# Kernel optimization log

Hardware: AMD Instinct MI355X
Metric: run time of the kernel (lower is better)

Reference implementation:

```python
import jax, jax.numpy as jnp
import numpy as np

S = 4096      # packed sequence length
DIM = 1024    # model dim
H = 8         # num heads
HD = 64       # per-branch head dim (head_dim // 2 in the module)
LAMBDA_INIT = 0.8 - 0.6 * float(np.exp(-0.3 * 0.0))  # depth=0 -> 0.2
EPS = 1e-5


def setup_inputs() -> dict:
    key = jax.random.key(0)
    ks = jax.random.split(key, 10)
    P = 2 * H * HD  # = 1024
    return {
        "x": jax.random.normal(ks[0], (S, DIM), jnp.float32),
        "mask": jnp.ones((1, 1, S, S), jnp.bool_),
        "Wq": jax.random.normal(ks[1], (DIM, P), jnp.float32) * 0.02,
        "Wk": jax.random.normal(ks[2], (DIM, P), jnp.float32) * 0.02,
        "Wv": jax.random.normal(ks[3], (DIM, P), jnp.float32) * 0.02,
        "Wo": jax.random.normal(ks[4], (P, DIM), jnp.float32) * 0.02,
        "lambda_q1": jax.random.normal(ks[5], (HD,), jnp.float32) * 0.1,
        "lambda_k1": jax.random.normal(ks[6], (HD,), jnp.float32) * 0.1,
        "lambda_q2": jax.random.normal(ks[7], (HD,), jnp.float32) * 0.1,
        "lambda_k2": jax.random.normal(ks[8], (HD,), jnp.float32) * 0.1,
        "subln_weight": jnp.ones((2 * HD,), jnp.float32),
    }


def reference(x, mask, Wq, Wk, Wv, Wo, lambda_q1, lambda_k1, lambda_q2,
              lambda_k2, subln_weight):
    # projections: (S, 2H, HD) split into branch index along a new axis
    xq = (x @ Wq).reshape(S, H, 2, HD)   # [2*H] view -> (H,2) contiguous split
    xk = (x @ Wk).reshape(S, H, 2, HD)
    xv = (x @ Wv).reshape(S, H, 2 * HD)
    q1, q2 = xq[:, :, 0], xq[:, :, 1]    # (S,H,HD)
    k1, k2 = xk[:, :, 0], xk[:, :, 1]

    scale = 1.0 / jnp.sqrt(jnp.float32(HD))
    bias = jnp.where(mask[0, 0], 0.0, -jnp.inf)  # (S,S) additive mask

    def sdpa(q, k):
        # q,k: (S,H,HD); xv: (S,H,2HD)
        scores = jnp.einsum('shd,thd->hst', q, k) * scale + bias  # (H,S,S)
        p = jax.nn.softmax(scores, axis=-1)
        return jnp.einsum('hst,thd->shd', p, xv)                  # (S,H,2HD)

    attn1 = sdpa(q1, k1)
    attn2 = sdpa(q2, k2)

    lam1 = jnp.exp(jnp.sum(lambda_q1 * lambda_k1))
    lam2 = jnp.exp(jnp.sum(lambda_q2 * lambda_k2))
    lambda_full = lam1 - lam2 + LAMBDA_INIT

    attn = attn1 - lambda_full * attn2                            # (S,H,2HD)
    # RMSNorm over last dim (2*HD) with learnable weight
    attn = attn * jax.lax.rsqrt(jnp.mean(attn * attn, axis=-1, keepdims=True) + EPS)
    attn = attn * subln_weight
    attn = attn * (1.0 - LAMBDA_INIT)
    return attn.reshape(S, H * 2 * HD) @ Wo                       # (S, DIM)
```

## Files before the change

### kernel.cpp

```cpp
#include <hip/hip_runtime.h>
#include <hip/hip_bf16.h>
#include <type_traits>
#include <utility>


using bf16 = __hip_bfloat16;

static constexpr int SQ = 4096;
static constexpr int DM = 1024;
static constexpr float LAMB_INIT = 0.2f;
static constexpr float KSC = 0.18033688011112043f;

typedef float  f32x4    __attribute__((ext_vector_type(4)));
typedef short  s16x4    __attribute__((ext_vector_type(4)));
typedef short  bf16x8_i __attribute__((ext_vector_type(8)));
typedef __bf16 bf16x8_b __attribute__((ext_vector_type(8)));

template<typename T, typename = void> struct mfma_ok : std::false_type {};
template<typename T> struct mfma_ok<T, std::void_t<decltype(
    __builtin_amdgcn_mfma_f32_16x16x32_bf16(std::declval<T>(), std::declval<T>(),
                                            std::declval<f32x4>(), 0, 0, 0))>>
    : std::true_type {};
using abfrag = std::conditional_t<mfma_ok<bf16x8_b>::value, bf16x8_b, bf16x8_i>;

__device__ __forceinline__ f32x4 mfma16(abfrag a, abfrag b, f32x4 c) {
    return __builtin_amdgcn_mfma_f32_16x16x32_bf16(a, b, c, 0, 0, 0);
}
__device__ __forceinline__ abfrag ldfrag(const bf16* p) {
    return *reinterpret_cast<const abfrag*>(p);
}
__device__ __forceinline__ short bf2s(bf16 b) {
    short s; __builtin_memcpy(&s, &b, 2); return s;
}
__device__ __forceinline__ float fexp2(float x) {
#if __has_builtin(__builtin_amdgcn_exp2f)
    return __builtin_amdgcn_exp2f(x);
#else
    return exp2f(x);
#endif
}
__device__ __forceinline__ int cvtpk(float lo, float hi) {
    int r;
    asm("v_cvt_pk_bf16_f32 %0, %1, %2" : "=v"(r) : "v"(lo), "v"(hi));
    return r;
}
__device__ __forceinline__ void gld_lds16(const bf16* g, bf16* l) {
    __builtin_amdgcn_global_load_lds((__attribute__((address_space(1))) void*)g,
                                     (__attribute__((address_space(3))) void*)l,
                                     16, 0, 0);
}


__global__ __launch_bounds__(256) void convert_x(const float* __restrict__ in,
                                                 bf16* __restrict__ outp)
{
    const size_t i = ((size_t)blockIdx.x * 256 + threadIdx.x) * 4;
    const f32x4 v = *reinterpret_cast<const f32x4*>(in + i);
    s16x4 o;
#pragma unroll
    for (int j = 0; j < 4; ++j) o[j] = bf2s(__float2bfloat16(v[j]));
    *reinterpret_cast<s16x4*>(outp + i) = o;
}

__global__ __launch_bounds__(256) void transpose_w(
    const float* __restrict__ Wq, const float* __restrict__ Wk,
    const float* __restrict__ Wv, const float* __restrict__ Wo,
    bf16* __restrict__ Wqt, bf16* __restrict__ Wkt,
    bf16* __restrict__ Wvt, bf16* __restrict__ Wot)
{
    const int z = blockIdx.z;
    const float* src = (z == 0) ? Wq : (z == 1) ? Wk : (z == 2) ? Wv : Wo;
    bf16* dst        = (z == 0) ? Wqt : (z == 1) ? Wkt : (z == 2) ? Wvt : Wot;
    const float scale = (z == 0) ? KSC : 1.0f;
    __shared__ float tbuf[32][33];
    const int k0 = blockIdx.x * 32, n0 = blockIdx.y * 32;
    const int c = threadIdx.x & 31, r0 = threadIdx.x >> 5;
#pragma unroll
    for (int i = 0; i < 4; ++i)
        tbuf[r0 + i * 8][c] = src[(size_t)(k0 + r0 + i * 8) * 1024 + n0 + c];
    __syncthreads();
#pragma unroll
    for (int i = 0; i < 4; ++i)
        dst[(size_t)(n0 + r0 + i * 8) * 1024 + k0 + c] =
            __float2bfloat16(tbuf[c][r0 + i * 8] * scale);
}

__global__ __launch_bounds__(256) void transpose_v(const bf16* __restrict__ V,
                                                   bf16* __restrict__ Vt)
{
    __shared__ bf16 tbuf[32][33];
    const int s0 = blockIdx.x * 32, n0 = blockIdx.y * 32;
    const int c = threadIdx.x & 31, r0 = threadIdx.x >> 5;
#pragma unroll
    for (int i = 0; i < 4; ++i)
        tbuf[r0 + i * 8][c] = V[(size_t)(s0 + r0 + i * 8) * 1024 + n0 + c];
    __syncthreads();
#pragma unroll
    for (int i = 0; i < 4; ++i)
        Vt[(size_t)(n0 + r0 + i * 8) * 4096 + s0 + c] = tbuf[c][r0 + i * 8];
}

__global__ void lambda_kernel(const float* lq1, const float* lk1,
                              const float* lq2, const float* lk2, float* outp)
{
    const int lane = threadIdx.x;
    float a = lq1[lane] * lk1[lane];
    float b = lq2[lane] * lk2[lane];
#pragma unroll
    for (int m = 1; m < 64; m <<= 1) {
        a += __shfl_xor(a, m, 64);
        b += __shfl_xor(b, m, 64);
    }
    if (lane == 0) outp[0] = __expf(a) - __expf(b) + LAMB_INIT;
}


template<bool BF16OUT>
__device__ __forceinline__ void gemm_core(const bf16* __restrict__ A,
                                          const bf16* __restrict__ Bt,
                                          void* __restrict__ Cout,
                                          int m0, int n0, int ldc)
{
    __shared__ __align__(16) bf16 As[128 * 32];
    __shared__ __align__(16) bf16 Bs[128 * 32];
    const int tid  = threadIdx.x;
    const int wid  = tid >> 6;
    const int lane = tid & 63;
    const int l15  = lane & 15;
    const int l4   = lane >> 4;
    const int wr   = wid >> 1;
    const int wc   = wid & 1;

    const f32x4 zero4 = {0.f, 0.f, 0.f, 0.f};
    f32x4 acc[4][4];
#pragma unroll
    for (int i = 0; i < 4; ++i)
#pragma unroll
        for (int j = 0; j < 4; ++j) acc[i][j] = zero4;

    for (int kt = 0; kt < 1024; kt += 32) {
        __syncthreads();
#pragma unroll
        for (int it = 0; it < 2; ++it) {
            const int flat = it * 256 + tid;
            const int row  = flat >> 2;
            const int c16  = flat & 3;
            const int ldst = (it * 256 + wid * 64) * 8;
            gld_lds16(&A [(size_t)(m0 + row) * 1024 + kt + c16 * 8], &As[ldst]);
            gld_lds16(&Bt[(size_t)(n0 + row) * 1024 + kt + c16 * 8], &Bs[ldst]);
        }
        __syncthreads();
        abfrag a[4], b[4];
#pragma unroll
        for (int mi = 0; mi < 4; ++mi)
            a[mi] = ldfrag(&As[(wr * 64 + mi * 16 + l15) * 32 + l4 * 8]);
#pragma unroll
        for (int ni = 0; ni < 4; ++ni)
            b[ni] = ldfrag(&Bs[(wc * 64 + ni * 16 + l15) * 32 + l4 * 8]);
#pragma unroll
        for (int mi = 0; mi < 4; ++mi)
#pragma unroll
            for (int ni = 0; ni < 4; ++ni)
                acc[mi][ni] = mfma16(a[mi], b[ni], acc[mi][ni]);
    }

#pragma unroll
    for (int mi = 0; mi < 4; ++mi)
#pragma unroll
        for (int ni = 0; ni < 4; ++ni)
#pragma unroll
            for (int r = 0; r < 4; ++r) {
                const int row = m0 + wr * 64 + mi * 16 + l4 * 4 + r;
                const int col = n0 + wc * 64 + ni * 16 + l15;
                if constexpr (BF16OUT)
                    ((bf16*)Cout)[(size_t)row * ldc + col] = __float2bfloat16(acc[mi][ni][r]);
                else
                    ((float*)Cout)[(size_t)row * ldc + col] = acc[mi][ni][r];
            }
}

__global__ __launch_bounds__(256, 2) void gemm_qkv(
    const bf16* __restrict__ xbf,
    const bf16* __restrict__ Wqt, const bf16* __restrict__ Wkt,
    const bf16* __restrict__ Wvt,
    bf16* __restrict__ Qo, bf16* __restrict__ Ko, bf16* __restrict__ Vo)
{
    const int which = blockIdx.y >> 3;
    const bf16* Bt = (which == 0) ? Wqt : (which == 1) ? Wkt : Wvt;
    bf16* Cp       = (which == 0) ? Qo  : (which == 1) ? Ko  : Vo;
    gemm_core<true>(xbf, Bt, Cp, blockIdx.x * 128, (blockIdx.y & 7) * 128, 1024);
}

__global__ __launch_bounds__(256, 2) void gemm_out(
    const bf16* __restrict__ Amat, const bf16* __restrict__ Wot,
    float* __restrict__ out)
{
    gemm_core<false>(Amat, Wot, out, blockIdx.x * 128, blockIdx.y * 128, 1024);
}


__global__ __launch_bounds__(512, 2) void flash_diff(
    const bf16* __restrict__ Qm, const bf16* __restrict__ Km,
    const bf16* __restrict__ Vtm, const float* __restrict__ lam_ptr,
    const float* __restrict__ subln, bf16* __restrict__ Amat)
{
    const int bid  = blockIdx.x;
    const int h    = bid & 7;
    const int qt   = bid >> 3;
    const int tid  = threadIdx.x;
    const int wid  = tid >> 6;
    const int lane = tid & 63;
    const int l15  = lane & 15;
    const int l4   = lane >> 4;
    const int qbase = qt * 128 + wid * 16;
    const int swz   = (l15 & 7) << 4;

    constexpr float THR = 8.0f;
    constexpr int KOFF = 0, VOFF = 49152, BUFSZ = 16384;

    __shared__ __align__(16) char smem[98304];

    abfrag qf[2][2];
#pragma unroll
    for (int c = 0; c < 2; ++c)
#pragma unroll
        for (int kc = 0; kc < 2; ++kc)
            qf[c][kc] = ldfrag(&Qm[(size_t)(qbase + l15) * DM +
                                   h * 128 + c * 64 + kc * 32 + l4 * 8]);
    asm volatile("" :: "v"(qf[0][0]), "v"(qf[0][1]), "v"(qf[1][0]), "v"(qf[1][1]));

    union { abfrag f; short s[8]; } uon;
#pragma unroll
    for (int i = 0; i < 8; ++i) uon.s[i] = (short)0x3F80;
    const abfrag ones = uon.f;

    const bf16* kap[2];
    const bf16* vap[2];
#pragma unroll
    for (int it = 0; it < 2; ++it) {
        const int slot = it * 512 + tid;
        const int krow = slot >> 4;
        const int kcb  = ((slot & 15) << 4) ^ ((krow & 7) << 4);
        kap[it] = Km + (size_t)krow * DM + h * 128 + (kcb >> 1);
        const int vrow = slot >> 3;
        const int vcb  = ((slot & 7) << 4) ^ ((vrow & 7) << 4);
        vap[it] = Vtm + (size_t)(h * 128 + vrow) * SQ + (vcb >> 1);
    }
    auto stage = [&](int buf) {
        char* kd = smem + KOFF + buf * BUFSZ;
        char* vd = smem + VOFF + buf * BUFSZ;
#pragma unroll
        for (int it = 0; it < 2; ++it) {
            gld_lds16(kap[it], (bf16*)(kd + (it * 512 + wid * 64) * 16));
            kap[it] += 64 * DM;
            gld_lds16(vap[it], (bf16*)(vd + (it * 512 + wid * 64) * 16));
            vap[it] += 64;
        }
    };

    const int kLane0 = l15 * 256 + ((l4 * 16) ^ swz);
    const int kLane1 = l15 * 256 + ((64 + l4 * 16) ^ swz);
    int vLane[4];
#pragma unroll
    for (int ch = 0; ch < 2; ++ch)
#pragma unroll
        for (int hh = 0; hh < 2; ++hh)
            vLane[ch * 2 + hh] = l15 * 128 + ((ch * 64 + hh * 32 + l4 * 8) ^ swz);

    const f32x4 zero4 = {0.f, 0.f, 0.f, 0.f};
    f32x4 o_[2][8];
#pragma unroll
    for (int c = 0; c < 2; ++c)
#pragma unroll
        for (int vt = 0; vt < 8; ++vt) o_[c][vt] = zero4;
    f32x4 lacc[2] = {zero4, zero4};
    float m_loc[2] = {0.f, 0.f};

    stage(0);
    stage(1);
    asm volatile("s_waitcnt vmcnt(4)" ::: "memory");
    __builtin_amdgcn_s_barrier();

    int cur = 0, nxt = 2;
    constexpr int NT = SQ / 64;
#pragma unroll 1
    for (int t = 0; t < NT; ++t) {
        const bool pf = (t + 2 < NT);
        if (pf) stage(nxt);

        const char* kbuf = smem + KOFF + cur * BUFSZ;
        const char* vbuf = smem + VOFF + cur * BUFSZ;
        const char* kb0  = kbuf + kLane0;
        const char* kb1  = kbuf + kLane1;

        abfrag pa[2][2];
#pragma unroll
        for (int c = 0; c < 2; ++c) {
            const float mc = m_loc[c];
            const f32x4 binit = {-mc, -mc, -mc, -mc};
            f32x4 sc[4];
#pragma unroll
            for (int j = 0; j < 4; ++j) {
                const abfrag k0 = *(const abfrag*)(kb0 + (j * 4096 + c * 128));
                const abfrag k1 = *(const abfrag*)(kb1 + (j * 4096 + c * 128));
                f32x4 z = mfma16(k0, qf[c][0], binit);
                sc[j] = mfma16(k1, qf[c][1], z);
            }
            float lmx = fmaxf(fmaxf(sc[0][0], sc[0][1]), fmaxf(sc[0][2], sc[0][3]));
#pragma unroll
            for (int j = 1; j < 4; ++j)
                lmx = fmaxf(lmx, fmaxf(fmaxf(sc[j][0], sc[j][1]),
                                       fmaxf(sc[j][2], sc[j][3])));
            if (__any(lmx > THR)) {
                float mx = lmx;
                mx = fmaxf(mx, __shfl_xor(mx, 16, 64));
                mx = fmaxf(mx, __shfl_xor(mx, 32, 64));
                const float alpha = fexp2(-mx);
                m_loc[c] += mx;
#pragma unroll
                for (int r = 0; r < 4; ++r) {
                    const float alr = __shfl(alpha, l4 * 4 + r, 64);
#pragma unroll
                    for (int vt = 0; vt < 8; ++vt) o_[c][vt][r] *= alr;
                    lacc[c][r] *= alr;
                }
#pragma unroll
                for (int j = 0; j < 4; ++j)
#pragma unroll
                    for (int r = 0; r < 4; ++r) sc[j][r] -= mx;
            }
            f32x4 pe[4];
#pragma unroll
            for (int j = 0; j < 4; ++j)
#pragma unroll
                for (int r = 0; r < 4; ++r) pe[j][r] = fexp2(sc[j][r]);
            union { abfrag f; int i[4]; } u0, u1;
            u0.i[0] = cvtpk(pe[0][0], pe[0][1]);
            u0.i[1] = cvtpk(pe[0][2], pe[0][3]);
            u0.i[2] = cvtpk(pe[1][0], pe[1][1]);
            u0.i[3] = cvtpk(pe[1][2], pe[1][3]);
            u1.i[0] = cvtpk(pe[2][0], pe[2][1]);
            u1.i[1] = cvtpk(pe[2][2], pe[2][3]);
            u1.i[2] = cvtpk(pe[3][0], pe[3][1]);
            u1.i[3] = cvtpk(pe[3][2], pe[3][3]);
            pa[c][0] = u0.f;
            pa[c][1] = u1.f;
        }

        const char* vb00 = vbuf + vLane[0];
        const char* vb01 = vbuf + vLane[1];
        const char* vb10 = vbuf + vLane[2];
        const char* vb11 = vbuf + vLane[3];

        __builtin_amdgcn_s_setprio(1);
        lacc[0] = mfma16(pa[0][0], ones, lacc[0]);
        lacc[0] = mfma16(pa[0][1], ones, lacc[0]);
        lacc[1] = mfma16(pa[1][0], ones, lacc[1]);
        lacc[1] = mfma16(pa[1][1], ones, lacc[1]);
#pragma unroll
        for (int vt = 0; vt < 8; ++vt) {
            union { abfrag f; s16x4 hh[2]; } v0, v1;
            v0.hh[0] = *(const s16x4*)(vb00 + vt * 2048);
            v0.hh[1] = *(const s16x4*)(vb01 + vt * 2048);
            v1.hh[0] = *(const s16x4*)(vb10 + vt * 2048);
            v1.hh[1] = *(const s16x4*)(vb11 + vt * 2048);
            o_[0][vt] = mfma16(pa[0][0], v0.f, o_[0][vt]);
            o_[1][vt] = mfma16(pa[1][0], v0.f, o_[1][vt]);
            o_[0][vt] = mfma16(pa[0][1], v1.f, o_[0][vt]);
            o_[1][vt] = mfma16(pa[1][1], v1.f, o_[1][vt]);
        }
        __builtin_amdgcn_s_setprio(0);

        if (pf) asm volatile("s_waitcnt vmcnt(4)" ::: "memory");
        else    asm volatile("s_waitcnt vmcnt(0)" ::: "memory");
        __builtin_amdgcn_s_barrier();
        cur = (cur == 2) ? 0 : cur + 1;
        nxt = (nxt == 2) ? 0 : nxt + 1;
    }

    const float lam = lam_ptr[0];
    float il1[4], il2[4];
#pragma unroll
    for (int r = 0; r < 4; ++r) {
        il1[r] = 1.f / lacc[0][r];
        il2[r] = lam / lacc[1][r];
    }
#pragma unroll
    for (int r = 0; r < 4; ++r) {
        float comb[8];
        float ss = 0.f;
#pragma unroll
        for (int vt = 0; vt < 8; ++vt) {
            const float v = o_[0][vt][r] * il1[r] - o_[1][vt][r] * il2[r];
            comb[vt] = v;
            ss += v * v;
        }
        ss += __shfl_xor(ss, 1, 64);
        ss += __shfl_xor(ss, 2, 64);
        ss += __shfl_xor(ss, 4, 64);
        ss += __shfl_xor(ss, 8, 64);
        const float rinv = rsqrtf(ss * (1.f / 128.f) + 1e-5f);
        const int row = qbase + l4 * 4 + r;
#pragma unroll
        for (int vt = 0; vt < 8; ++vt) {
            const float outv = comb[vt] * rinv * subln[vt * 16 + l15] * 0.8f;
            Amat[(size_t)row * DM + h * 128 + vt * 16 + l15] = __float2bfloat16(outv);
        }
    }
}


extern "C" void kernel_launch(void* const* d_in, const int* in_sizes, int n_in,
                              void* d_out, int out_size, void* d_ws, size_t ws_size,
                              hipStream_t stream)
{
    (void)in_sizes; (void)n_in; (void)out_size; (void)ws_size;
    const float* x    = (const float*)d_in[0];
    const float* Wq   = (const float*)d_in[2];
    const float* Wk   = (const float*)d_in[3];
    const float* Wv   = (const float*)d_in[4];
    const float* Wo   = (const float*)d_in[5];
    const float* lq1  = (const float*)d_in[6];
    const float* lk1  = (const float*)d_in[7];
    const float* lq2  = (const float*)d_in[8];
    const float* lk2  = (const float*)d_in[9];
    const float* subw = (const float*)d_in[10];

    char* ws = (char*)d_ws;
    size_t off = 0;
    auto take = [&](size_t n) { void* p = ws + off; off += (n + 255) & ~(size_t)255; return p; };
    bf16* xbf = (bf16*)take((size_t)SQ * DM * 2);
    bf16* Wqt = (bf16*)take((size_t)DM * DM * 2);
    bf16* Wkt = (bf16*)take((size_t)DM * DM * 2);
    bf16* Wvt = (bf16*)take((size_t)DM * DM * 2);
    bf16* Wot = (bf16*)take((size_t)DM * DM * 2);
    bf16* Qb  = (bf16*)take((size_t)SQ * DM * 2);
    bf16* Kb  = (bf16*)take((size_t)SQ * DM * 2);
    bf16* Vb  = (bf16*)take((size_t)SQ * DM * 2);
    bf16* Vtb = (bf16*)take((size_t)SQ * DM * 2);
    bf16* Am  = (bf16*)take((size_t)SQ * DM * 2);
    float* lamp = (float*)take(256);

    convert_x   <<<dim3(SQ * DM / 1024), dim3(256), 0, stream>>>(x, xbf);
    transpose_w <<<dim3(32, 32, 4),      dim3(256), 0, stream>>>(Wq, Wk, Wv, Wo, Wqt, Wkt, Wvt, Wot);
    lambda_kernel<<<dim3(1),             dim3(64),  0, stream>>>(lq1, lk1, lq2, lk2, lamp);
    gemm_qkv    <<<dim3(32, 24),         dim3(256), 0, stream>>>(xbf, Wqt, Wkt, Wvt, Qb, Kb, Vb);
    transpose_v <<<dim3(128, 32),        dim3(256), 0, stream>>>(Vb, Vtb);
    flash_diff  <<<dim3(256),            dim3(512), 0, stream>>>(Qb, Kb, Vtb, lamp, subw, Am);
    gemm_out    <<<dim3(32, 8),          dim3(256), 0, stream>>>(Am, Wot, (float*)d_out);
}
```

Before: 192.8 us.

## Split differential attention branches across separate waves in flash kernel

Each block now runs 16 waves instead of 8. Each pair of waves shares a 16-row query slice, and each wave of the pair handles one of the two attention branches (q1/k1 or q2/k2), so it holds half the accumulators. Each thread now issues one K and one V staging load per tile instead of two. Branch 2's normalized output is handed to branch 1's wave through LDS for the final combine and RMSNorm. This cuts per-wave register pressure and serial work to gain latency hiding, at the cost of an extra LDS exchange, a block-wide sync, and a launch bound of 1024 threads with min 4 blocks that may force register spills.

```diff
diff --git a/kernel.cpp b/kernel.cpp
--- a/kernel.cpp
+++ b/kernel.cpp
@@ -199,7 +199,7 @@
 }
 
 
-__global__ __launch_bounds__(512, 2) void flash_diff(
+__global__ __launch_bounds__(1024, 4) void flash_diff(
     const bf16* __restrict__ Qm, const bf16* __restrict__ Km,
     const bf16* __restrict__ Vtm, const float* __restrict__ lam_ptr,
     const float* __restrict__ subln, bf16* __restrict__ Amat)
@@ -212,7 +212,9 @@
     const int lane = tid & 63;
     const int l15  = lane & 15;
     const int l4   = lane >> 4;
-    const int qbase = qt * 128 + wid * 16;
+    const int qw   = wid >> 1;
+    const int cw   = wid & 1;
+    const int qbase = qt * 128 + qw * 16;
     const int swz   = (l15 & 7) << 4;
 
     constexpr float THR = 8.0f;
@@ -220,46 +222,34 @@
 
     __shared__ __align__(16) char smem[98304];
 
-    abfrag qf[2][2];
-#pragma unroll
-    for (int c = 0; c < 2; ++c)
-#pragma unroll
-        for (int kc = 0; kc < 2; ++kc)
-            qf[c][kc] = ldfrag(&Qm[(size_t)(qbase + l15) * DM +
-                                   h * 128 + c * 64 + kc * 32 + l4 * 8]);
-    asm volatile("" :: "v"(qf[0][0]), "v"(qf[0][1]), "v"(qf[1][0]), "v"(qf[1][1]));
+    abfrag qf[2];
+#pragma unroll
+    for (int kc = 0; kc < 2; ++kc)
+        qf[kc] = ldfrag(&Qm[(size_t)(qbase + l15) * DM +
+                            h * 128 + cw * 64 + kc * 32 + l4 * 8]);
+    asm volatile("" :: "v"(qf[0]), "v"(qf[1]));
 
     union { abfrag f; short s[8]; } uon;
 #pragma unroll
     for (int i = 0; i < 8; ++i) uon.s[i] = (short)0x3F80;
     const abfrag ones = uon.f;
 
-    const bf16* kap[2];
-    const bf16* vap[2];
-#pragma unroll
-    for (int it = 0; it < 2; ++it) {
-        const int slot = it * 512 + tid;
-        const int krow = slot >> 4;
-        const int kcb  = ((slot & 15) << 4) ^ ((krow & 7) << 4);
-        kap[it] = Km + (size_t)krow * DM + h * 128 + (kcb >> 1);
-        const int vrow = slot >> 3;
-        const int vcb  = ((slot & 7) << 4) ^ ((vrow & 7) << 4);
-        vap[it] = Vtm + (size_t)(h * 128 + vrow) * SQ + (vcb >> 1);
-    }
+    const int krow = tid >> 4;
+    const int kcb  = ((tid & 15) << 4) ^ ((krow & 7) << 4);
+    const bf16* kap = Km + (size_t)krow * DM + h * 128 + (kcb >> 1);
+    const int vrow = tid >> 3;
+    const int vcb  = ((tid & 7) << 4) ^ ((vrow & 7) << 4);
+    const bf16* vap = Vtm + (size_t)(h * 128 + vrow) * SQ + (vcb >> 1);
+
     auto stage = [&](int buf) {
-        char* kd = smem + KOFF + buf * BUFSZ;
-        char* vd = smem + VOFF + buf * BUFSZ;
-#pragma unroll
-        for (int it = 0; it < 2; ++it) {
-            gld_lds16(kap[it], (bf16*)(kd + (it * 512 + wid * 64) * 16));
-            kap[it] += 64 * DM;
-            gld_lds16(vap[it], (bf16*)(vd + (it * 512 + wid * 64) * 16));
-            vap[it] += 64;
-        }
+        gld_lds16(kap, (bf16*)(smem + KOFF + buf * BUFSZ + wid * 1024));
+        kap += 64 * DM;
+        gld_lds16(vap, (bf16*)(smem + VOFF + buf * BUFSZ + wid * 1024));
+        vap += 64;
     };
 
-    const int kLane0 = l15 * 256 + ((l4 * 16) ^ swz);
-    const int kLane1 = l15 * 256 + ((64 + l4 * 16) ^ swz);
+    const int kLane0 = l15 * 256 + ((l4 * 16) ^ swz) + cw * 128;
+    const int kLane1 = l15 * 256 + ((64 + l4 * 16) ^ swz) + cw * 128;
     int vLane[4];
 #pragma unroll
     for (int ch = 0; ch < 2; ++ch)
@@ -268,17 +258,15 @@
             vLane[ch * 2 + hh] = l15 * 128 + ((ch * 64 + hh * 32 + l4 * 8) ^ swz);
 
     const f32x4 zero4 = {0.f, 0.f, 0.f, 0.f};
-    f32x4 o_[2][8];
-#pragma unroll
-    for (int c = 0; c < 2; ++c)
-#pragma unroll
-        for (int vt = 0; vt < 8; ++vt) o_[c][vt] = zero4;
-    f32x4 lacc[2] = {zero4, zero4};
-    float m_loc[2] = {0.f, 0.f};
+    f32x4 o_[8];
+#pragma unroll
+    for (int vt = 0; vt < 8; ++vt) o_[vt] = zero4;
+    f32x4 lacc = zero4;
+    float m_loc = 0.f;
 
     stage(0);
     stage(1);
-    asm volatile("s_waitcnt vmcnt(4)" ::: "memory");
+    asm volatile("s_waitcnt vmcnt(2)" ::: "memory");
     __builtin_amdgcn_s_barrier();
 
     int cur = 0, nxt = 2;
@@ -293,47 +281,46 @@
         const char* kb0  = kbuf + kLane0;
         const char* kb1  = kbuf + kLane1;
 
-        abfrag pa[2][2];
-#pragma unroll
-        for (int c = 0; c < 2; ++c) {
-            const float mc = m_loc[c];
-            const f32x4 binit = {-mc, -mc, -mc, -mc};
-            f32x4 sc[4];
-#pragma unroll
-            for (int j = 0; j < 4; ++j) {
-                const abfrag k0 = *(const abfrag*)(kb0 + (j * 4096 + c * 128));
-                const abfrag k1 = *(const abfrag*)(kb1 + (j * 4096 + c * 128));
-                f32x4 z = mfma16(k0, qf[c][0], binit);
-                sc[j] = mfma16(k1, qf[c][1], z);
+        const float mc = m_loc;
+        const f32x4 binit = {-mc, -mc, -mc, -mc};
+        f32x4 sc[4];
+#pragma unroll
+        for (int j = 0; j < 4; ++j) {
+            const abfrag k0 = *(const abfrag*)(kb0 + j * 4096);
+            const abfrag k1 = *(const abfrag*)(kb1 + j * 4096);
+            f32x4 z = mfma16(k0, qf[0], binit);
+            sc[j] = mfma16(k1, qf[1], z);
+        }
+        float lmx = fmaxf(fmaxf(sc[0][0], sc[0][1]), fmaxf(sc[0][2], sc[0][3]));
+#pragma unroll
+        for (int j = 1; j < 4; ++j)
+            lmx = fmaxf(lmx, fmaxf(fmaxf(sc[j][0], sc[j][1]),
+                                   fmaxf(sc[j][2], sc[j][3])));
+        if (__any(lmx > THR)) {
+            float mx = lmx;
+            mx = fmaxf(mx, __shfl_xor(mx, 16, 64));
+            mx = fmaxf(mx, __shfl_xor(mx, 32, 64));
+            const float alpha = fexp2(-mx);
+            m_loc += mx;
+#pragma unroll
+            for (int r = 0; r < 4; ++r) {
+                const float alr = __shfl(alpha, l4 * 4 + r, 64);
+#pragma unroll
+                for (int vt = 0; vt < 8; ++vt) o_[vt][r] *= alr;
+                lacc[r] *= alr;
             }
-            float lmx = fmaxf(fmaxf(sc[0][0], sc[0][1]), fmaxf(sc[0][2], sc[0][3]));
-#pragma unroll
-            for (int j = 1; j < 4; ++j)
-                lmx = fmaxf(lmx, fmaxf(fmaxf(sc[j][0], sc[j][1]),
-                                       fmaxf(sc[j][2], sc[j][3])));
-            if (__any(lmx > THR)) {
-                float mx = lmx;
-                mx = fmaxf(mx, __shfl_xor(mx, 16, 64));
-                mx = fmaxf(mx, __shfl_xor(mx, 32, 64));
-                const float alpha = fexp2(-mx);
-                m_loc[c] += mx;
-#pragma unroll
-                for (int r = 0; r < 4; ++r) {
-                    const float alr = __shfl(alpha, l4 * 4 + r, 64);
-#pragma unroll
-                    for (int vt = 0; vt < 8; ++vt) o_[c][vt][r] *= alr;
-                    lacc[c][r] *= alr;
-                }
-#pragma unroll
-                for (int j = 0; j < 4; ++j)
-#pragma unroll
-                    for (int r = 0; r < 4; ++r) sc[j][r] -= mx;
-            }
-            f32x4 pe[4];
 #pragma unroll
             for (int j = 0; j < 4; ++j)
 #pragma unroll
-                for (int r = 0; r < 4; ++r) pe[j][r] = fexp2(sc[j][r]);
+                for (int r = 0; r < 4; ++r) sc[j][r] -= mx;
+        }
+        f32x4 pe[4];
+#pragma unroll
+        for (int j = 0; j < 4; ++j)
+#pragma unroll
+            for (int r = 0; r < 4; ++r) pe[j][r] = fexp2(sc[j][r]);
+        abfrag pa[2];
+        {
             union { abfrag f; int i[4]; } u0, u1;
             u0.i[0] = cvtpk(pe[0][0], pe[0][1]);
             u0.i[1] = cvtpk(pe[0][2], pe[0][3]);
@@ -343,8 +330,8 @@
             u1.i[1] = cvtpk(pe[2][2], pe[2][3]);
             u1.i[2] = cvtpk(pe[3][0], pe[3][1]);
             u1.i[3] = cvtpk(pe[3][2], pe[3][3]);
-            pa[c][0] = u0.f;
-            pa[c][1] = u1.f;
+            pa[0] = u0.f;
+            pa[1] = u1.f;
         }
 
         const char* vb00 = vbuf + vLane[0];
@@ -353,10 +340,8 @@
         const char* vb11 = vbuf + vLane[3];
 
         __builtin_amdgcn_s_setprio(1);
-        lacc[0] = mfma16(pa[0][0], ones, lacc[0]);
-        lacc[0] = mfma16(pa[0][1], ones, lacc[0]);
-        lacc[1] = mfma16(pa[1][0], ones, lacc[1]);
-        lacc[1] = mfma16(pa[1][1], ones, lacc[1]);
+        lacc = mfma16(pa[0], ones, lacc);
+        lacc = mfma16(pa[1], ones, lacc);
 #pragma unroll
         for (int vt = 0; vt < 8; ++vt) {
             union { abfrag f; s16x4 hh[2]; } v0, v1;
@@ -364,14 +349,12 @@
             v0.hh[1] = *(const s16x4*)(vb01 + vt * 2048);
             v1.hh[0] = *(const s16x4*)(vb10 + vt * 2048);
             v1.hh[1] = *(const s16x4*)(vb11 + vt * 2048);
-            o_[0][vt] = mfma16(pa[0][0], v0.f, o_[0][vt]);
-            o_[1][vt] = mfma16(pa[1][0], v0.f, o_[1][vt]);
-            o_[0][vt] = mfma16(pa[0][1], v1.f, o_[0][vt]);
-            o_[1][vt] = mfma16(pa[1][1], v1.f, o_[1][vt]);
+            o_[vt] = mfma16(pa[0], v0.f, o_[vt]);
+            o_[vt] = mfma16(pa[1], v1.f, o_[vt]);
         }
         __builtin_amdgcn_s_setprio(0);
 
-        if (pf) asm volatile("s_waitcnt vmcnt(4)" ::: "memory");
+        if (pf) asm volatile("s_waitcnt vmcnt(2)" ::: "memory");
         else    asm volatile("s_waitcnt vmcnt(0)" ::: "memory");
         __builtin_amdgcn_s_barrier();
         cur = (cur == 2) ? 0 : cur + 1;
@@ -379,32 +362,46 @@
     }
 
     const float lam = lam_ptr[0];
-    float il1[4], il2[4];
-#pragma unroll
-    for (int r = 0; r < 4; ++r) {
-        il1[r] = 1.f / lacc[0][r];
-        il2[r] = lam / lacc[1][r];
+    float* xch = (float*)smem;
+
+    if (cw == 1) {
+        float il2[4];
+#pragma unroll
+        for (int r = 0; r < 4; ++r) il2[r] = lam / lacc[r];
+#pragma unroll
+        for (int vt = 0; vt < 8; ++vt)
+#pragma unroll
+            for (int r = 0; r < 4; ++r)
+                xch[(qw * 16 + l4 * 4 + r) * 128 + vt * 16 + l15] =
+                    o_[vt][r] * il2[r];
     }
-#pragma unroll
-    for (int r = 0; r < 4; ++r) {
-        float comb[8];
-        float ss = 0.f;
-#pragma unroll
-        for (int vt = 0; vt < 8; ++vt) {
-            const float v = o_[0][vt][r] * il1[r] - o_[1][vt][r] * il2[r];
-            comb[vt] = v;
-            ss += v * v;
-        }
-        ss += __shfl_xor(ss, 1, 64);
-        ss += __shfl_xor(ss, 2, 64);
-        ss += __shfl_xor(ss, 4, 64);
-        ss += __shfl_xor(ss, 8, 64);
-        const float rinv = rsqrtf(ss * (1.f / 128.f) + 1e-5f);
-        const int row = qbase + l4 * 4 + r;
-#pragma unroll
-        for (int vt = 0; vt < 8; ++vt) {
-            const float outv = comb[vt] * rinv * subln[vt * 16 + l15] * 0.8f;
-            Amat[(size_t)row * DM + h * 128 + vt * 16 + l15] = __float2bfloat16(outv);
+    __syncthreads();
+    if (cw == 0) {
+        float il1[4];
+#pragma unroll
+        for (int r = 0; r < 4; ++r) il1[r] = 1.f / lacc[r];
+#pragma unroll
+        for (int r = 0; r < 4; ++r) {
+            float comb[8];
+            float ss = 0.f;
+#pragma unroll
+            for (int vt = 0; vt < 8; ++vt) {
+                const float v = o_[vt][r] * il1[r] -
+                                xch[(qw * 16 + l4 * 4 + r) * 128 + vt * 16 + l15];
+                comb[vt] = v;
+                ss += v * v;
+            }
+            ss += __shfl_xor(ss, 1, 64);
+            ss += __shfl_xor(ss, 2, 64);
+            ss += __shfl_xor(ss, 4, 64);
+            ss += __shfl_xor(ss, 8, 64);
+            const float rinv = rsqrtf(ss * (1.f / 128.f) + 1e-5f);
+            const int row = qbase + l4 * 4 + r;
+#pragma unroll
+            for (int vt = 0; vt < 8; ++vt) {
+                const float outv = comb[vt] * rinv * subln[vt * 16 + l15] * 0.8f;
+                Amat[(size_t)row * DM + h * 128 + vt * 16 + l15] = __float2bfloat16(outv);
+            }
         }
     }
 }
@@ -446,6 +443,6 @@
     lambda_kernel<<<dim3(1),             dim3(64),  0, stream>>>(lq1, lk1, lq2, lk2, lamp);
     gemm_qkv    <<<dim3(32, 24),         dim3(256), 0, stream>>>(xbf, Wqt, Wkt, Wvt, Qb, Kb, Vb);
     transpose_v <<<dim3(128, 32),        dim3(256), 0, stream>>>(Vb, Vtb);
-    flash_diff  <<<dim3(256),            dim3(512), 0, stream>>>(Qb, Kb, Vtb, lamp, subw, Am);
+    flash_diff  <<<dim3(256),            dim3(1024), 0, stream>>>(Qb, Kb, Vtb, lamp, subw, Am);
     gemm_out    <<<dim3(32, 8),          dim3(256), 0, stream>>>(Am, Wot, (float*)d_out);
 }
```

Measured after the change: 235.7 us. 22.2% more time.

## Split attention over KV halves with 32-row query tiles and a combine kernel

Applied to the files above, without the earlier changes.

Each warp of the flash kernel now handles 32 query rows instead of 16, so every K/V tile staged in shared memory feeds twice as many MFMAs. The grid stays at 256 blocks because the key sequence is split into two halves (split-K). Each block writes unnormalized partial outputs in bf16 plus per-row sums and running maxima. A new combine kernel merges the two halves, applies the lambda difference and RMSNorm, and writes the activation matrix. This adds extra global traffic for the partials, one more launch, and roughly doubled accumulator registers per thread, which risks spills at the 512-thread, 2-block launch bound.

```diff
diff --git a/kernel.cpp b/kernel.cpp
--- a/kernel.cpp
+++ b/kernel.cpp
@@ -201,18 +201,21 @@
 
 __global__ __launch_bounds__(512, 2) void flash_diff(
     const bf16* __restrict__ Qm, const bf16* __restrict__ Km,
-    const bf16* __restrict__ Vtm, const float* __restrict__ lam_ptr,
-    const float* __restrict__ subln, bf16* __restrict__ Amat)
+    const bf16* __restrict__ Vtm,
+    bf16* __restrict__ pO,
+    float* __restrict__ pL,
+    float* __restrict__ pM)
 {
     const int bid  = blockIdx.x;
     const int h    = bid & 7;
-    const int qt   = bid >> 3;
+    const int qt   = (bid >> 3) & 15;
+    const int ks   = bid >> 7;
     const int tid  = threadIdx.x;
     const int wid  = tid >> 6;
     const int lane = tid & 63;
     const int l15  = lane & 15;
     const int l4   = lane >> 4;
-    const int qbase = qt * 128 + wid * 16;
+    const int qbase = qt * 256 + wid * 32;
     const int swz   = (l15 & 7) << 4;
 
     constexpr float THR = 8.0f;
@@ -220,14 +223,16 @@
 
     __shared__ __align__(16) char smem[98304];
 
-    abfrag qf[2][2];
-#pragma unroll
-    for (int c = 0; c < 2; ++c)
-#pragma unroll
-        for (int kc = 0; kc < 2; ++kc)
-            qf[c][kc] = ldfrag(&Qm[(size_t)(qbase + l15) * DM +
-                                   h * 128 + c * 64 + kc * 32 + l4 * 8]);
-    asm volatile("" :: "v"(qf[0][0]), "v"(qf[0][1]), "v"(qf[1][0]), "v"(qf[1][1]));
+    abfrag qf[2][2][2];
+#pragma unroll
+    for (int sub = 0; sub < 2; ++sub)
+#pragma unroll
+        for (int c = 0; c < 2; ++c)
+#pragma unroll
+            for (int kc = 0; kc < 2; ++kc)
+                qf[sub][c][kc] = ldfrag(&Qm[(size_t)(qbase + sub * 16 + l15) * DM +
+                                            h * 128 + c * 64 + kc * 32 + l4 * 8]);
+    asm volatile("" :: "v"(qf[0][0][0]), "v"(qf[1][1][1]));
 
     union { abfrag f; short s[8]; } uon;
 #pragma unroll
@@ -241,10 +246,10 @@
         const int slot = it * 512 + tid;
         const int krow = slot >> 4;
         const int kcb  = ((slot & 15) << 4) ^ ((krow & 7) << 4);
-        kap[it] = Km + (size_t)krow * DM + h * 128 + (kcb >> 1);
+        kap[it] = Km + (size_t)(ks * 2048 + krow) * DM + h * 128 + (kcb >> 1);
         const int vrow = slot >> 3;
         const int vcb  = ((slot & 7) << 4) ^ ((vrow & 7) << 4);
-        vap[it] = Vtm + (size_t)(h * 128 + vrow) * SQ + (vcb >> 1);
+        vap[it] = Vtm + (size_t)(h * 128 + vrow) * SQ + ks * 2048 + (vcb >> 1);
     }
     auto stage = [&](int buf) {
         char* kd = smem + KOFF + buf * BUFSZ;
@@ -268,13 +273,15 @@
             vLane[ch * 2 + hh] = l15 * 128 + ((ch * 64 + hh * 32 + l4 * 8) ^ swz);
 
     const f32x4 zero4 = {0.f, 0.f, 0.f, 0.f};
-    f32x4 o_[2][8];
-#pragma unroll
-    for (int c = 0; c < 2; ++c)
-#pragma unroll
-        for (int vt = 0; vt < 8; ++vt) o_[c][vt] = zero4;
-    f32x4 lacc[2] = {zero4, zero4};
-    float m_loc[2] = {0.f, 0.f};
+    f32x4 o_[2][2][8];
+#pragma unroll
+    for (int sub = 0; sub < 2; ++sub)
+#pragma unroll
+        for (int c = 0; c < 2; ++c)
+#pragma unroll
+            for (int vt = 0; vt < 8; ++vt) o_[sub][c][vt] = zero4;
+    f32x4 lacc[2][2] = {{zero4, zero4}, {zero4, zero4}};
+    float m_loc[2][2] = {{0.f, 0.f}, {0.f, 0.f}};
 
     stage(0);
     stage(1);
@@ -282,7 +289,7 @@
     __builtin_amdgcn_s_barrier();
 
     int cur = 0, nxt = 2;
-    constexpr int NT = SQ / 64;
+    constexpr int NT = 2048 / 64;
 #pragma unroll 1
     for (int t = 0; t < NT; ++t) {
         const bool pf = (t + 2 < NT);
@@ -293,18 +300,20 @@
         const char* kb0  = kbuf + kLane0;
         const char* kb1  = kbuf + kLane1;
 
-        abfrag pa[2][2];
+        abfrag pa[2][2][2];
+#pragma unroll
+        for (int sub = 0; sub < 2; ++sub)
 #pragma unroll
         for (int c = 0; c < 2; ++c) {
-            const float mc = m_loc[c];
+            const float mc = m_loc[sub][c];
             const f32x4 binit = {-mc, -mc, -mc, -mc};
             f32x4 sc[4];
 #pragma unroll
             for (int j = 0; j < 4; ++j) {
                 const abfrag k0 = *(const abfrag*)(kb0 + (j * 4096 + c * 128));
                 const abfrag k1 = *(const abfrag*)(kb1 + (j * 4096 + c * 128));
-                f32x4 z = mfma16(k0, qf[c][0], binit);
-                sc[j] = mfma16(k1, qf[c][1], z);
+                f32x4 z = mfma16(k0, qf[sub][c][0], binit);
+                sc[j] = mfma16(k1, qf[sub][c][1], z);
             }
             float lmx = fmaxf(fmaxf(sc[0][0], sc[0][1]), fmaxf(sc[0][2], sc[0][3]));
 #pragma unroll
@@ -316,35 +325,34 @@
                 mx = fmaxf(mx, __shfl_xor(mx, 16, 64));
                 mx = fmaxf(mx, __shfl_xor(mx, 32, 64));
                 const float alpha = fexp2(-mx);
-                m_loc[c] += mx;
+                m_loc[sub][c] += mx;
 #pragma unroll
                 for (int r = 0; r < 4; ++r) {
                     const float alr = __shfl(alpha, l4 * 4 + r, 64);
 #pragma unroll
-                    for (int vt = 0; vt < 8; ++vt) o_[c][vt][r] *= alr;
-                    lacc[c][r] *= alr;
+                    for (int vt = 0; vt < 8; ++vt) o_[sub][c][vt][r] *= alr;
+                    lacc[sub][c][r] *= alr;
                 }
 #pragma unroll
                 for (int j = 0; j < 4; ++j)
 #pragma unroll
                     for (int r = 0; r < 4; ++r) sc[j][r] -= mx;
             }
-            f32x4 pe[4];
 #pragma unroll
             for (int j = 0; j < 4; ++j)
 #pragma unroll
-                for (int r = 0; r < 4; ++r) pe[j][r] = fexp2(sc[j][r]);
+                for (int r = 0; r < 4; ++r) sc[j][r] = fexp2(sc[j][r]);
             union { abfrag f; int i[4]; } u0, u1;
-            u0.i[0] = cvtpk(pe[0][0], pe[0][1]);
-            u0.i[1] = cvtpk(pe[0][2], pe[0][3]);
-            u0.i[2] = cvtpk(pe[1][0], pe[1][1]);
-            u0.i[3] = cvtpk(pe[1][2], pe[1][3]);
-            u1.i[0] = cvtpk(pe[2][0], pe[2][1]);
-            u1.i[1] = cvtpk(pe[2][2], pe[2][3]);
-            u1.i[2] = cvtpk(pe[3][0], pe[3][1]);
-            u1.i[3] = cvtpk(pe[3][2], pe[3][3]);
-            pa[c][0] = u0.f;
-            pa[c][1] = u1.f;
+            u0.i[0] = cvtpk(sc[0][0], sc[0][1]);
+            u0.i[1] = cvtpk(sc[0][2], sc[0][3]);
+            u0.i[2] = cvtpk(sc[1][0], sc[1][1]);
+            u0.i[3] = cvtpk(sc[1][2], sc[1][3]);
+            u1.i[0] = cvtpk(sc[2][0], sc[2][1]);
+            u1.i[1] = cvtpk(sc[2][2], sc[2][3]);
+            u1.i[2] = cvtpk(sc[3][0], sc[3][1]);
+            u1.i[3] = cvtpk(sc[3][2], sc[3][3]);
+            pa[sub][c][0] = u0.f;
+            pa[sub][c][1] = u1.f;
         }
 
         const char* vb00 = vbuf + vLane[0];
@@ -353,10 +361,13 @@
         const char* vb11 = vbuf + vLane[3];
 
         __builtin_amdgcn_s_setprio(1);
-        lacc[0] = mfma16(pa[0][0], ones, lacc[0]);
-        lacc[0] = mfma16(pa[0][1], ones, lacc[0]);
-        lacc[1] = mfma16(pa[1][0], ones, lacc[1]);
-        lacc[1] = mfma16(pa[1][1], ones, lacc[1]);
+#pragma unroll
+        for (int sub = 0; sub < 2; ++sub)
+#pragma unroll
+            for (int c = 0; c < 2; ++c) {
+                lacc[sub][c] = mfma16(pa[sub][c][0], ones, lacc[sub][c]);
+                lacc[sub][c] = mfma16(pa[sub][c][1], ones, lacc[sub][c]);
+            }
 #pragma unroll
         for (int vt = 0; vt < 8; ++vt) {
             union { abfrag f; s16x4 hh[2]; } v0, v1;
@@ -364,10 +375,13 @@
             v0.hh[1] = *(const s16x4*)(vb01 + vt * 2048);
             v1.hh[0] = *(const s16x4*)(vb10 + vt * 2048);
             v1.hh[1] = *(const s16x4*)(vb11 + vt * 2048);
-            o_[0][vt] = mfma16(pa[0][0], v0.f, o_[0][vt]);
-            o_[1][vt] = mfma16(pa[1][0], v0.f, o_[1][vt]);
-            o_[0][vt] = mfma16(pa[0][1], v1.f, o_[0][vt]);
-            o_[1][vt] = mfma16(pa[1][1], v1.f, o_[1][vt]);
+#pragma unroll
+            for (int sub = 0; sub < 2; ++sub)
+#pragma unroll
+                for (int c = 0; c < 2; ++c) {
+                    o_[sub][c][vt] = mfma16(pa[sub][c][0], v0.f, o_[sub][c][vt]);
+                    o_[sub][c][vt] = mfma16(pa[sub][c][1], v1.f, o_[sub][c][vt]);
+                }
         }
         __builtin_amdgcn_s_setprio(0);
 
@@ -378,35 +392,72 @@
         nxt = (nxt == 2) ? 0 : nxt + 1;
     }
 
+#pragma unroll
+    for (int sub = 0; sub < 2; ++sub)
+#pragma unroll
+        for (int c = 0; c < 2; ++c) {
+            const size_t plane = (size_t)(ks * 2 + c);
+#pragma unroll
+            for (int vt = 0; vt < 8; ++vt)
+#pragma unroll
+                for (int r = 0; r < 4; ++r) {
+                    const int row = qbase + sub * 16 + l4 * 4 + r;
+                    pO[(plane * SQ + row) * 1024 + h * 128 + vt * 16 + l15] =
+                        __float2bfloat16(o_[sub][c][vt][r]);
+                }
+            if (l15 == 0)
+#pragma unroll
+                for (int r = 0; r < 4; ++r)
+                    pL[(plane * 8 + h) * SQ + qbase + sub * 16 + l4 * 4 + r] =
+                        lacc[sub][c][r];
+            if (l4 == 0)
+                pM[(plane * 8 + h) * SQ + qbase + sub * 16 + l15] = m_loc[sub][c];
+        }
+}
+
+
+__global__ __launch_bounds__(256) void combine(
+    const bf16* __restrict__ pO, const float* __restrict__ pL,
+    const float* __restrict__ pM, const float* __restrict__ lam_ptr,
+    const float* __restrict__ subln, bf16* __restrict__ Amat)
+{
+    const int row  = blockIdx.x * 4 + (threadIdx.x >> 6);
+    const int q    = row >> 3;
+    const int h    = row & 7;
+    const int lane = threadIdx.x & 63;
+    const int col  = lane * 2;
     const float lam = lam_ptr[0];
-    float il1[4], il2[4];
-#pragma unroll
-    for (int r = 0; r < 4; ++r) {
-        il1[r] = 1.f / lacc[0][r];
-        il2[r] = lam / lacc[1][r];
+
+    float n1[2], n2[2];
+#pragma unroll
+    for (int c = 0; c < 2; ++c) {
+        const size_t pa = (size_t)(0 * 2 + c), pb = (size_t)(1 * 2 + c);
+        const float ma = pM[(pa * 8 + h) * SQ + q];
+        const float mb = pM[(pb * 8 + h) * SQ + q];
+        const float m  = fmaxf(ma, mb);
+        const float aa = fexp2(ma - m), ab = fexp2(mb - m);
+        const float l  = aa * pL[(pa * 8 + h) * SQ + q] +
+                         ab * pL[(pb * 8 + h) * SQ + q];
+        const unsigned wa = *(const unsigned*)(pO + (pa * SQ + q) * 1024 + h * 128 + col);
+        const unsigned wb = *(const unsigned*)(pO + (pb * SQ + q) * 1024 + h * 128 + col);
+        const float oa0 = __uint_as_float(wa << 16);
+        const float oa1 = __uint_as_float(wa & 0xffff0000u);
+        const float ob0 = __uint_as_float(wb << 16);
+        const float ob1 = __uint_as_float(wb & 0xffff0000u);
+        const float il = 1.0f / l;
+        float* dst = (c == 0) ? n1 : n2;
+        dst[0] = (aa * oa0 + ab * ob0) * il;
+        dst[1] = (aa * oa1 + ab * ob1) * il;
     }
-#pragma unroll
-    for (int r = 0; r < 4; ++r) {
-        float comb[8];
-        float ss = 0.f;
-#pragma unroll
-        for (int vt = 0; vt < 8; ++vt) {
-            const float v = o_[0][vt][r] * il1[r] - o_[1][vt][r] * il2[r];
-            comb[vt] = v;
-            ss += v * v;
-        }
-        ss += __shfl_xor(ss, 1, 64);
-        ss += __shfl_xor(ss, 2, 64);
-        ss += __shfl_xor(ss, 4, 64);
-        ss += __shfl_xor(ss, 8, 64);
-        const float rinv = rsqrtf(ss * (1.f / 128.f) + 1e-5f);
-        const int row = qbase + l4 * 4 + r;
-#pragma unroll
-        for (int vt = 0; vt < 8; ++vt) {
-            const float outv = comb[vt] * rinv * subln[vt * 16 + l15] * 0.8f;
-            Amat[(size_t)row * DM + h * 128 + vt * 16 + l15] = __float2bfloat16(outv);
-        }
-    }
+    const float v0 = n1[0] - lam * n2[0];
+    const float v1 = n1[1] - lam * n2[1];
+    float ss = v0 * v0 + v1 * v1;
+#pragma unroll
+    for (int m = 1; m < 64; m <<= 1) ss += __shfl_xor(ss, m, 64);
+    const float rinv = rsqrtf(ss * (1.0f / 128.f) + 1e-5f);
+    const float o0 = v0 * rinv * subln[col] * 0.8f;
+    const float o1 = v1 * rinv * subln[col + 1] * 0.8f;
+    *(int*)(Amat + (size_t)q * 1024 + h * 128 + col) = cvtpk(o0, o1);
 }
 
 
@@ -439,6 +490,9 @@
     bf16* Vb  = (bf16*)take((size_t)SQ * DM * 2);
     bf16* Vtb = (bf16*)take((size_t)SQ * DM * 2);
     bf16* Am  = (bf16*)take((size_t)SQ * DM * 2);
+    bf16* pO  = (bf16*)take((size_t)4 * SQ * DM * 2);
+    float* pL = (float*)take((size_t)4 * 8 * SQ * 4);
+    float* pM = (float*)take((size_t)4 * 8 * SQ * 4);
     float* lamp = (float*)take(256);
 
     convert_x   <<<dim3(SQ * DM / 1024), dim3(256), 0, stream>>>(x, xbf);
@@ -446,6 +500,7 @@
     lambda_kernel<<<dim3(1),             dim3(64),  0, stream>>>(lq1, lk1, lq2, lk2, lamp);
     gemm_qkv    <<<dim3(32, 24),         dim3(256), 0, stream>>>(xbf, Wqt, Wkt, Wvt, Qb, Kb, Vb);
     transpose_v <<<dim3(128, 32),        dim3(256), 0, stream>>>(Vb, Vtb);
-    flash_diff  <<<dim3(256),            dim3(512), 0, stream>>>(Qb, Kb, Vtb, lamp, subw, Am);
+    flash_diff  <<<dim3(256),            dim3(512), 0, stream>>>(Qb, Kb, Vtb, pO, pL, pM);
+    combine     <<<dim3(SQ * 8 / 4),     dim3(256), 0, stream>>>(pO, pL, pM, lamp, subw, Am);
     gemm_out    <<<dim3(32, 8),          dim3(256), 0, stream>>>(Am, Wot, (float*)d_out);
 }
```

Measured after the change: 198.9 us. 1.03x slower.
